# Performance work log

Measured on AMD Instinct MI355X. Metric: run time of the kernel, lower is better.

The kernel has to match this reference:

```python
import jax, jax.numpy as jnp
import numpy as np

_SIGMA = 1.5
_K1 = 0.01
_K2 = 0.03
WINDOW_SIZE = 11
VALUE_RANGE = 1.0


def gaussian_window(size: int, sigma: float) -> jnp.ndarray:
    # 1D gaussian, normalized; 2D window is the outer product (sums to 1)
    coords = jnp.arange(size, dtype=jnp.float32) - (size - 1) / 2.0
    g = jnp.exp(-(coords ** 2) / (2.0 * sigma ** 2))
    g = g / g.sum()
    return jnp.outer(g, g)  # (k, k)


def depthwise_conv(img, win2d):
    # img: (N, C, H, W), win2d: (k, k); depthwise valid conv, groups=C
    C = img.shape[1]
    kern = jnp.broadcast_to(win2d[:, :, None, None], win2d.shape + (1, C))  # HWIO
    return jax.lax.conv_general_dilated(
        img, kern, window_strides=(1, 1), padding='VALID',
        dimension_numbers=('NCHW', 'HWIO', 'NCHW'), feature_group_count=C)


def setup_inputs() -> dict:
    key = jax.random.key(0)
    k1, k2 = jax.random.split(key)
    x = jax.random.uniform(k1, (16, 3, 512, 512), dtype=jnp.float32)
    y = jax.random.uniform(k2, (16, 3, 512, 512), dtype=jnp.float32)
    window = gaussian_window(WINDOW_SIZE, _SIGMA)
    return {'x': x, 'y': y, 'window': window}


def reference(x, y, window):
    mu_x = depthwise_conv(x, window)
    mu_y = depthwise_conv(y, window)
    mu_x_sq = mu_x ** 2
    mu_y_sq = mu_y ** 2
    mu_xy = mu_x * mu_y
    sigma_x_sq = depthwise_conv(x * x, window) - mu_x_sq
    sigma_y_sq = depthwise_conv(y * y, window) - mu_y_sq
    sigma_xy = depthwise_conv(x * y, window) - mu_xy
    c1 = (_K1 * VALUE_RANGE) ** 2
    c2 = (_K2 * VALUE_RANGE) ** 2
    cs_map = (2.0 * sigma_xy + c2) / (sigma_x_sq + sigma_y_sq + c2)
    ssim_map = (2.0 * mu_xy + c1) / (mu_x_sq + mu_y_sq + c1) * cs_map
    # mean over spatial dims -> (N, C), mean over channels -> (N,), reduction='mean' -> scalar
    return ssim_map.mean(axis=(-1, -2)).mean(axis=-1).mean()
```

## Files before the change

### kernel.cpp

```cpp
#include <hip/hip_runtime.h>
#include <math.h>

#define KS    11
#define H     512
#define W     512
#define OH    502
#define OW    502
#define NPLANES 48
#define TOTAL_OUT (NPLANES * OH * OW)

#define TH      8
#define IROWS   (TH + KS - 1)
#define NSIG    4
#define LVW     523
#define NTHREADS 512
#define NCHUNKS 10
#define CROWS   51

__global__ void zero_out_kernel(float* out) { out[0] = 0.0f; }

__global__ __launch_bounds__(NTHREADS, 2) void ssim_kernel(
    const float* __restrict__ x,
    const float* __restrict__ y,
    const float* __restrict__ win,
    float* __restrict__ out)
{
    __shared__ float v[NSIG][TH][LVW];
    __shared__ float w1s[KS];
    __shared__ float wsum[NTHREADS / 64];

    const int t     = threadIdx.x;
    const int chunk = blockIdx.x;
    const int plane = blockIdx.y;

    const int row_lo = chunk * CROWS;
    const int row_hi = (row_lo + CROWS < OH) ? (row_lo + CROWS) : OH;
    const int niter  = (row_hi - row_lo + TH - 1) / TH;

    const float* __restrict__ xp = x + (size_t)plane * (H * W);
    const float* __restrict__ yp = y + (size_t)plane * (H * W);

    if (t < KS) w1s[t] = sqrtf(win[t * KS + t]);
    __syncthreads();

    float w[KS];
#pragma unroll
    for (int k = 0; k < KS; k++) w[k] = w1s[k];

    const int r  = t & 7;
    const int c0 = (t >> 3) << 3;
    const float c1 = 1e-4f;
    const float c2 = 9e-4f;
    float acc = 0.f;

    float rx[IROWS], ry[IROWS];
    {
#pragma unroll
        for (int j = 0; j < IROWS; j++) {
            int gy = row_lo + j; gy = (gy < H - 1) ? gy : (H - 1);
            rx[j] = xp[gy * W + t];
            ry[j] = yp[gy * W + t];
        }
    }

    for (int it = 0; it < niter; ++it) {
        const int gy0 = row_lo + it * TH;

        float a0[TH], a1[TH], a2[TH], a3[TH];
#pragma unroll
        for (int q = 0; q < TH; q++) { a0[q]=0.f; a1[q]=0.f; a2[q]=0.f; a3[q]=0.f; }

#pragma unroll
        for (int j = 0; j < IROWS; j++) {
            const float xv = rx[j], yv = ry[j];
            const float pss = xv * xv + yv * yv;
            const float pxy = xv * yv;
#pragma unroll
            for (int q = 0; q < TH; q++) {
                if (j - q >= 0 && j - q < KS) {
                    const float wk = w[j - q];
                    a0[q] += wk * xv;
                    a1[q] += wk * yv;
                    a2[q] += wk * pss;
                    a3[q] += wk * pxy;
                }
            }
        }

        __syncthreads();
#pragma unroll
        for (int q = 0; q < TH; q++) {
            v[0][q][t] = a0[q];
            v[1][q][t] = a1[q];
            v[2][q][t] = a2[q];
            v[3][q][t] = a3[q];
        }
        __syncthreads();

        if (it + 1 < niter) {
            const int ny0 = row_lo + (it + 1) * TH;
#pragma unroll
            for (int j = 0; j < IROWS; j++) {
                int gy = ny0 + j; gy = (gy < H - 1) ? gy : (H - 1);
                rx[j] = xp[gy * W + t];
                ry[j] = yp[gy * W + t];
            }
        }

        float mu[NSIG][TH];
#pragma unroll
        for (int s = 0; s < NSIG; s++) {
            const float* __restrict__ vrow = &v[s][r][c0];
            float vs[IROWS];
#pragma unroll
            for (int j = 0; j < IROWS; j++) vs[j] = vrow[j];
#pragma unroll
            for (int p = 0; p < TH; p++) {
                float m = 0.f;
#pragma unroll
                for (int k = 0; k < KS; k++) m += w[k] * vs[p + k];
                mu[s][p] = m;
            }
        }

        const int grow  = gy0 + r;
        const bool rowok = (grow < row_hi);
#pragma unroll
        for (int p = 0; p < TH; p++) {
            if (rowok && (c0 + p) < OW) {
                const float mux = mu[0][p], muy = mu[1][p];
                const float mxy = mux * muy;
                const float m2  = mux * mux + muy * muy;
                const float sss = mu[2][p] - m2;
                const float sxy = mu[3][p] - mxy;
                const float num = (2.f * sxy + c2) * (2.f * mxy + c1);
                const float den = (sss + c2) * (m2 + c1);
                acc += num * __builtin_amdgcn_rcpf(den);
            }
        }
    }

#pragma unroll
    for (int off = 32; off > 0; off >>= 1)
        acc += __shfl_down(acc, off, 64);

    if ((t & 63) == 0) wsum[t >> 6] = acc;
    __syncthreads();
    if (t == 0) {
        float s = 0.f;
#pragma unroll
        for (int i = 0; i < NTHREADS / 64; i++) s += wsum[i];
        atomicAdd(out, s * (1.0f / (float)TOTAL_OUT));
    }
}

extern "C" void kernel_launch(void* const* d_in, const int* in_sizes, int n_in,
                              void* d_out, int out_size, void* d_ws, size_t ws_size,
                              hipStream_t stream)
{
    const float* x   = (const float*)d_in[0];
    const float* y   = (const float*)d_in[1];
    const float* win = (const float*)d_in[2];
    float* out = (float*)d_out;

    zero_out_kernel<<<1, 1, 0, stream>>>(out);

    dim3 grid(NCHUNKS, NPLANES);
    ssim_kernel<<<grid, NTHREADS, 0, stream>>>(x, y, win, out);
}
```

Before: 161.6 us.

## Shrink row tile to 4, use 32-row chunks, drop register prefetch for occupancy

Halves the per-iteration row tile (TH 8→4) and splits each plane into 16 chunks of 32 rows instead of 10 chunks of 51. It removes the software prefetch of the next tile's input rows and raises the launch-bounds minimum from 2 to 3 blocks, aiming to cut register and shared-memory pressure and give more blocks for latency hiding. In exchange, the vertical halo overhead per output row rises (14 input rows for 4 output rows instead of 18 for 8), the horizontal pass does more redundant loads, and global-load latency is no longer overlapped with compute inside a block.

```diff
diff --git a/kernel.cpp b/kernel.cpp
--- a/kernel.cpp
+++ b/kernel.cpp
@@ -9,17 +9,18 @@
 #define NPLANES 48
 #define TOTAL_OUT (NPLANES * OH * OW)
 
-#define TH      8
+#define TH      4
 #define IROWS   (TH + KS - 1)
 #define NSIG    4
 #define LVW     523
 #define NTHREADS 512
-#define NCHUNKS 10
-#define CROWS   51
+#define CHUNK   32
+#define ITERS   (CHUNK / TH)
+#define NCHUNKS 16
 
 __global__ void zero_out_kernel(float* out) { out[0] = 0.0f; }
 
-__global__ __launch_bounds__(NTHREADS, 2) void ssim_kernel(
+__global__ __launch_bounds__(NTHREADS, 3) void ssim_kernel(
     const float* __restrict__ x,
     const float* __restrict__ y,
     const float* __restrict__ win,
@@ -33,9 +34,8 @@
     const int chunk = blockIdx.x;
     const int plane = blockIdx.y;
 
-    const int row_lo = chunk * CROWS;
-    const int row_hi = (row_lo + CROWS < OH) ? (row_lo + CROWS) : OH;
-    const int niter  = (row_hi - row_lo + TH - 1) / TH;
+    const int row_lo = chunk * CHUNK;
+    const int row_hi = (row_lo + CHUNK < OH) ? (row_lo + CHUNK) : OH;
 
     const float* __restrict__ xp = x + (size_t)plane * (H * W);
     const float* __restrict__ yp = y + (size_t)plane * (H * W);
@@ -47,24 +47,23 @@
 #pragma unroll
     for (int k = 0; k < KS; k++) w[k] = w1s[k];
 
-    const int r  = t & 7;
-    const int c0 = (t >> 3) << 3;
+    const int r  = t & 3;
+    const int c0 = (t >> 2) << 2;
     const float c1 = 1e-4f;
     const float c2 = 9e-4f;
     float acc = 0.f;
 
-    float rx[IROWS], ry[IROWS];
-    {
+    for (int it = 0; it < ITERS; ++it) {
+        const int gy0 = row_lo + it * TH;
+        if (gy0 >= row_hi) break;
+
+        float rxv[IROWS], ryv[IROWS];
 #pragma unroll
         for (int j = 0; j < IROWS; j++) {
-            int gy = row_lo + j; gy = (gy < H - 1) ? gy : (H - 1);
-            rx[j] = xp[gy * W + t];
-            ry[j] = yp[gy * W + t];
+            int gy = gy0 + j; gy = (gy < H - 1) ? gy : (H - 1);
+            rxv[j] = xp[gy * W + t];
+            ryv[j] = yp[gy * W + t];
         }
-    }
-
-    for (int it = 0; it < niter; ++it) {
-        const int gy0 = row_lo + it * TH;
 
         float a0[TH], a1[TH], a2[TH], a3[TH];
 #pragma unroll
@@ -72,7 +71,7 @@
 
 #pragma unroll
         for (int j = 0; j < IROWS; j++) {
-            const float xv = rx[j], yv = ry[j];
+            const float xv = rxv[j], yv = ryv[j];
             const float pss = xv * xv + yv * yv;
             const float pxy = xv * yv;
 #pragma unroll
@@ -96,16 +95,6 @@
             v[3][q][t] = a3[q];
         }
         __syncthreads();
-
-        if (it + 1 < niter) {
-            const int ny0 = row_lo + (it + 1) * TH;
-#pragma unroll
-            for (int j = 0; j < IROWS; j++) {
-                int gy = ny0 + j; gy = (gy < H - 1) ? gy : (H - 1);
-                rx[j] = xp[gy * W + t];
-                ry[j] = yp[gy * W + t];
-            }
-        }
 
         float mu[NSIG][TH];
 #pragma unroll
```

After: 165.4 us. +2.4%, slower.
